# Performance work log

Hardware: AMD Instinct MI355X
Metric: run time of the kernel (lower is better)

The kernel has to match this reference:

```python
import jax, jax.numpy as jnp
import numpy as np

B, L, H, W = 64, 512, 768, 255


def setup_inputs() -> dict:
    key = jax.random.key(0)
    k1, k2 = jax.random.split(key)
    sequence_output = jax.random.normal(k1, (B, L, H), dtype=jnp.float32)
    # subword lengths in {1,2}; W=255 guarantees cumsum <= 510 <= L-1 (CLS at pos 0)
    words_lengths = jax.random.randint(k2, (B, W), 1, 3, dtype=jnp.int32)
    return {"sequence_output": sequence_output, "words_lengths": words_lengths}


def reference(sequence_output, words_lengths):
    # sequence_output: [B, L, H] (BERT last_hidden_state after dropout=identity in eval)
    # words_lengths:   [B, W] number of subword tokens per word (0 => padding word)
    Bv, Lv, Hv = sequence_output.shape
    Wv = words_lengths.shape[1]

    cls_output = sequence_output[:, 0, :]  # [B, H]

    # word w occupies tokens [starts[w], ends[w]) with starts = 1 + cumsum - len
    ends = 1 + jnp.cumsum(words_lengths, axis=1)  # [B, W]
    tok = jnp.arange(Lv)                          # [L]

    # token t belongs to word i iff ends[i-1] <= t < ends[i]; zero-length words are
    # skipped automatically by searchsorted(side='right') on the nondecreasing ends.
    word_id = jax.vmap(lambda e: jnp.searchsorted(e, tok, side="right"))(ends)  # [B, L]

    valid = (tok[None, :] >= 1) & (word_id < Wv)  # exclude [CLS] and tokens past last word
    seg_id = jnp.where(valid, word_id, Wv)        # dump invalid tokens into segment W

    sums = jax.vmap(
        lambda x, s: jax.ops.segment_sum(x, s, num_segments=Wv + 1)
    )(sequence_output, seg_id)[:, :Wv]            # [B, W, H]

    denom = jnp.maximum(words_lengths, 1).astype(sequence_output.dtype)  # avoid /0
    context_embedding = sums / denom[..., None]
    context_embedding = jnp.where(
        (words_lengths > 0)[..., None], context_embedding, jnp.zeros((), sums.dtype)
    )
    return cls_output, context_embedding
```

## Files before the change

kernel.cpp:

```cpp
#include <hip/hip_runtime.h>

#define B_ 64
#define L_ 512
#define H_ 768
#define W_ 255
#define H4 (H_ / 4)

__global__ void scan_starts(const int* __restrict__ lengths, int* __restrict__ starts) {
    int b = blockIdx.x;
    const int* len = lengths + b * W_;
    int* st = starts + b * W_;
    int lane = threadIdx.x;
    int carry = 1;
    for (int base = 0; base < W_; base += 64) {
        int i = base + lane;
        int v = (i < W_) ? len[i] : 0;
        int s = v;
        #pragma unroll
        for (int off = 1; off < 64; off <<= 1) {
            int u = __shfl_up(s, off, 64);
            if (lane >= off) s += u;
        }
        if (i < W_) st[i] = carry + (s - v);
        carry += __shfl(s, 63, 64);
    }
}

__global__ __launch_bounds__(H4) void word_mean(
        const float* __restrict__ seq,
        const int* __restrict__ lengths,
        const int* __restrict__ starts,
        float* __restrict__ cls_out,
        float* __restrict__ ctx_out) {
    int w = blockIdx.x;
    int b = blockIdx.y;
    int t = threadIdx.x;
    const float4* base = (const float4*)(seq + (size_t)b * L_ * H_);

    if (w == W_) {
        ((float4*)cls_out)[(size_t)b * H4 + t] = base[t];
        return;
    }

    int len   = lengths[b * W_ + w];
    int start = starts [b * W_ + w];

    float4 acc = make_float4(0.f, 0.f, 0.f, 0.f);
    if (len > 0) {
        int end = start + len;
        if (end > L_) end = L_;
        for (int tok = start; tok < end; ++tok) {
            float4 v = base[(size_t)tok * H4 + t];
            acc.x += v.x; acc.y += v.y; acc.z += v.z; acc.w += v.w;
        }
        float inv = 1.0f / (float)len;
        acc.x *= inv; acc.y *= inv; acc.z *= inv; acc.w *= inv;
    }
    ((float4*)ctx_out)[((size_t)b * W_ + w) * H4 + t] = acc;
}

extern "C" void kernel_launch(void* const* d_in, const int* in_sizes, int n_in,
                              void* d_out, int out_size, void* d_ws, size_t ws_size,
                              hipStream_t stream) {
    const float* seq     = (const float*)d_in[0];
    const int*   lengths = (const int*)d_in[1];

    float* cls_out = (float*)d_out;
    float* ctx_out = (float*)d_out + (size_t)B_ * H_;

    int* starts = (int*)d_ws;

    scan_starts<<<B_, 64, 0, stream>>>(lengths, starts);

    dim3 grid(W_ + 1, B_);
    word_mean<<<grid, H4, 0, stream>>>(seq, lengths, starts, cls_out, ctx_out);
}
```

Measured before the change: 159.5 us.

## Fuse prefix scan into word-mean kernel and process 16 words per block

```diff
diff --git a/kernel.cpp b/kernel.cpp
--- a/kernel.cpp
+++ b/kernel.cpp
@@ -5,58 +5,65 @@
 #define H_ 768
 #define W_ 255
 #define H4 (H_ / 4)
+#define WPB 16
+#define NCHUNK 16
 
-__global__ void scan_starts(const int* __restrict__ lengths, int* __restrict__ starts) {
-    int b = blockIdx.x;
+__global__ __launch_bounds__(H4) void wordrep_fused(
+        const float* __restrict__ seq,
+        const int* __restrict__ lengths,
+        float* __restrict__ cls_out,
+        float* __restrict__ ctx_out) {
+    int chunk = blockIdx.x;
+    int b     = blockIdx.y;
+    int t     = threadIdx.x;
+    const float4* base = (const float4*)(seq + (size_t)b * L_ * H_);
+
+    if (chunk == NCHUNK) {
+        ((float4*)cls_out)[(size_t)b * H4 + t] = base[t];
+        return;
+    }
+
+    int w0 = chunk * WPB;
+    int nw = min(WPB, W_ - w0);
+    int lane = t & 63;
     const int* len = lengths + b * W_;
-    int* st = starts + b * W_;
-    int lane = threadIdx.x;
+
+    int myStart = 0, myLen = 0;
     int carry = 1;
-    for (int base = 0; base < W_; base += 64) {
-        int i = base + lane;
-        int v = (i < W_) ? len[i] : 0;
+    int lim = w0 + nw;
+    for (int basew = 0; basew < lim; basew += 64) {
+        int i = basew + lane;
+        int v = (i < lim) ? len[i] : 0;
         int s = v;
         #pragma unroll
         for (int off = 1; off < 64; off <<= 1) {
             int u = __shfl_up(s, off, 64);
             if (lane >= off) s += u;
         }
-        if (i < W_) st[i] = carry + (s - v);
+        if (i >= w0 && i < lim) { myStart = carry + (s - v); myLen = v; }
         carry += __shfl(s, 63, 64);
     }
-}
 
-__global__ __launch_bounds__(H4) void word_mean(
-        const float* __restrict__ seq,
-        const int* __restrict__ lengths,
-        const int* __restrict__ starts,
-        float* __restrict__ cls_out,
-        float* __restrict__ ctx_out) {
-    int w = blockIdx.x;
-    int b = blockIdx.y;
-    int t = threadIdx.x;
-    const float4* base = (const float4*)(seq + (size_t)b * L_ * H_);
+    int srcBase = w0 & 63;
+    float4* out = (float4*)ctx_out + ((size_t)b * W_ + w0) * H4 + t;
 
-    if (w == W_) {
-        ((float4*)cls_out)[(size_t)b * H4 + t] = base[t];
-        return;
+    #pragma unroll 4
+    for (int j = 0; j < nw; ++j) {
+        int sj = __shfl(myStart, srcBase + j, 64);
+        int lj = __shfl(myLen,  srcBase + j, 64);
+        float4 acc = make_float4(0.f, 0.f, 0.f, 0.f);
+        if (lj > 0) {
+            int end = sj + lj;
+            if (end > L_) end = L_;
+            for (int tok = sj; tok < end; ++tok) {
+                float4 v = base[(size_t)tok * H4 + t];
+                acc.x += v.x; acc.y += v.y; acc.z += v.z; acc.w += v.w;
+            }
+            float inv = 1.0f / (float)lj;
+            acc.x *= inv; acc.y *= inv; acc.z *= inv; acc.w *= inv;
+        }
+        out[(size_t)j * H4] = acc;
     }
-
-    int len   = lengths[b * W_ + w];
-    int start = starts [b * W_ + w];
-
-    float4 acc = make_float4(0.f, 0.f, 0.f, 0.f);
-    if (len > 0) {
-        int end = start + len;
-        if (end > L_) end = L_;
-        for (int tok = start; tok < end; ++tok) {
-            float4 v = base[(size_t)tok * H4 + t];
-            acc.x += v.x; acc.y += v.y; acc.z += v.z; acc.w += v.w;
-        }
-        float inv = 1.0f / (float)len;
-        acc.x *= inv; acc.y *= inv; acc.z *= inv; acc.w *= inv;
-    }
-    ((float4*)ctx_out)[((size_t)b * W_ + w) * H4 + t] = acc;
 }
 
 extern "C" void kernel_launch(void* const* d_in, const int* in_sizes, int n_in,
@@ -68,10 +75,6 @@
     float* cls_out = (float*)d_out;
     float* ctx_out = (float*)d_out + (size_t)B_ * H_;
 
-    int* starts = (int*)d_ws;
-
-    scan_starts<<<B_, 64, 0, stream>>>(lengths, starts);
-
-    dim3 grid(W_ + 1, B_);
-    word_mean<<<grid, H4, 0, stream>>>(seq, lengths, starts, cls_out, ctx_out);
+    dim3 grid(NCHUNK + 1, B_);
+    wordrep_fused<<<grid, H4, 0, stream>>>(seq, lengths, cls_out, ctx_out);
 }
```

Result: no change. 162.2 us (+1.7%).
